# Performance work log

Measured on AMD Instinct MI355X. Metric: run time of the kernel, lower is better.

## Reference

```python
import jax, jax.numpy as jnp
import numpy as np

B, S, D, H, V, DFF = 8, 1024, 768, 12, 50257, 3072


def setup_inputs() -> dict:
    key = jax.random.key(0)
    ks = jax.random.split(key, 10)
    return {
        "idx": jax.random.randint(ks[0], (B, S), 0, V),
        "wte": jax.random.normal(ks[1], (V, D), jnp.float32) * 0.2,
        "wpe": jax.random.normal(ks[2], (S + 1, D), jnp.float32) * 0.2,
        "wq_diag": jax.random.normal(ks[3], (H, D), jnp.float32) * 0.2,
        "wk_diag": jax.random.normal(ks[4], (H, D), jnp.float32) * 0.2,
        "wv_diag": jax.random.normal(ks[5], (H, D), jnp.float32) * 0.2,
        "w_lr": jax.random.normal(ks[6], (1, H, 1, 1), jnp.float32) * 0.01,
        "w_o": jax.random.normal(ks[7], (D, H * D), jnp.float32) * 0.02,
        "mlp_w1": jax.random.normal(ks[8], (DFF, D), jnp.float32) * 0.02,
        "mlp_w2": jax.random.normal(ks[9], (D, DFF), jnp.float32) * 0.02,
    }


def _forward(idx, wte, wpe, wq_diag, wk_diag, wv_diag, w_lr, w_o, mlp_w1, mlp_w2):
    b_sz, s = idx.shape
    e = wte[idx]                               # (B,S,D) token embeddings
    p = wpe[: s + 1]                           # (S+1,D) positions 0..S
    e_mean = jnp.mean(wte, axis=0)             # E_wte: mean embedding (D,)
    invn = 1.0 / (jnp.arange(s, dtype=e.dtype) + 1.0)  # diag of W_N

    # diag-mode projections: (x @ diag(w)) == x * w  (per head)
    q = p[1:][None] * wq_diag[:, None, :]      # (H,S,D) -- batch-independent
    k = p[:-1][None] * wk_diag[:, None, :]     # (H,S,D)
    v = (e - e_mean)[:, None] * wv_diag[None, :, None, :]  # (B,H,S,D)

    scores = jnp.einsum("hsd,htd->hst", q, k)  # (H,S,S), identical per batch
    mask = jnp.tril(jnp.ones((s, s), bool))
    scores = jnp.where(mask, scores, -jnp.inf)
    attn = jax.nn.softmax(scores, axis=-1)
    y = jnp.einsum("hst,bhtd->bhsd", attn, v)  # (B,H,S,D)

    y = y * invn[:, None]                      # W_N @ y (diagonal -> row scale)
    y = y * w_lr                               # per-head W_LR scale
    # torch does y.view(B, S, H*D) on a (B,H,S,D) tensor: raw memory reinterpret
    y = y.reshape(b_sz, s, H * D)
    y = y @ w_o.T                              # W_o proj -> (B,S,D)

    # b = W_N @ (e - E_wte); torch broadcast-matmul then sum over dim=1 == batch
    b_term = (e - e_mean) * invn[None, :, None]        # (B,S,D)
    y = y + jnp.sum(b_term, axis=0)[None]              # (1,S,D) broadcast add

    # FFN block: x = x + mlp(x), GELU exact, no bias, dropout=0
    x = y + jax.nn.gelu(y @ mlp_w1.T, approximate=False) @ mlp_w2.T

    # targets=None path: logits only for last position, tied lm_head = wte
    logits = x[:, -1:, :] @ wte.T              # (B,1,V)
    return logits


def reference(idx, wte, wpe, wq_diag, wk_diag, wv_diag, w_lr, w_o, mlp_w1, mlp_w2):
    return _forward(idx, wte, wpe, wq_diag, wk_diag, wv_diag, w_lr, w_o, mlp_w1, mlp_w2)
```

## Files before the change

kernel.cpp:

```cpp
#include <hip/hip_runtime.h>
#include <math.h>

#define B 8
#define S 1024
#define D 768
#define H 12
#define V 50257
#define DFF 3072
#define HD (H*D)
#define SLO 1012
#define NS 12

#define OFF_EMEAN 0
#define OFF_A     768
#define OFF_GQ    (OFF_A + B*NS*D)
#define OFF_SC    (OFF_GQ + NS*D)
#define OFF_YV    (OFF_SC + NS*S)
#define OFF_YO    (OFF_YV + B*HD)
#define OFF_G     (OFF_YO + B*D)
#define OFF_X     (OFF_G + B*DFF)

typedef float f4 __attribute__((ext_vector_type(4)));

__device__ __forceinline__ float wsum(float v) {
    v += __shfl_xor(v, 1, 64);
    v += __shfl_xor(v, 2, 64);
    v += __shfl_xor(v, 4, 64);
    v += __shfl_xor(v, 8, 64);
    v += __shfl_xor(v, 16, 64);
    v += __shfl_xor(v, 32, 64);
    return v;
}

#define K14_K4_BLOCKS 256
#define K14_K1_BLOCKS 512
#define K1_ROWS 99
__global__ __launch_bounds__(768) void k14_emean_accA(const int* __restrict__ idx,
                                                      const float* __restrict__ wte,
                                                      float* __restrict__ ws) {
    __shared__ float wl[32 * 12];
    const int bid = blockIdx.x;
    const int tid = threadIdx.x;
    if (bid >= K14_K4_BLOCKS) {
        const int kb = bid - K14_K4_BLOCKS;
        int r0 = kb * K1_ROWS;
        if (r0 >= V) return;
        int r1 = r0 + K1_ROWS; if (r1 > V) r1 = V;
        const float* __restrict__ p = wte + (size_t)r0 * D + tid;
        float a0 = 0.f, a1 = 0.f, a2 = 0.f, a3 = 0.f;
        int r = r0;
        for (; r + 8 <= r1; r += 8) {
            const float* q0 = p;
            const float* q1 = p + 1 * D;
            const float* q2 = p + 2 * D;
            const float* q3 = p + 3 * D;
            const float* q4 = p + 4 * D;
            const float* q5 = p + 5 * D;
            const float* q6 = p + 6 * D;
            const float* q7 = p + 7 * D;
            float t0, t1, t2, t3, t4, t5, t6, t7;
            asm volatile("global_load_dword %0, %1, off" : "=v"(t0) : "v"(q0));
            asm volatile("global_load_dword %0, %1, off" : "=v"(t1) : "v"(q1));
            asm volatile("global_load_dword %0, %1, off" : "=v"(t2) : "v"(q2));
            asm volatile("global_load_dword %0, %1, off" : "=v"(t3) : "v"(q3));
            asm volatile("global_load_dword %0, %1, off" : "=v"(t4) : "v"(q4));
            asm volatile("global_load_dword %0, %1, off" : "=v"(t5) : "v"(q5));
            asm volatile("global_load_dword %0, %1, off" : "=v"(t6) : "v"(q6));
            asm volatile("global_load_dword %0, %1, off" : "=v"(t7) : "v"(q7));
            asm volatile("s_waitcnt vmcnt(0)"
                         : "+v"(t0), "+v"(t1), "+v"(t2), "+v"(t3),
                           "+v"(t4), "+v"(t5), "+v"(t6), "+v"(t7)
                         :
                         : "memory");
            __builtin_amdgcn_sched_barrier(0);
            a0 += t0 + t4; a1 += t1 + t5; a2 += t2 + t6; a3 += t3 + t7;
            p += 8 * D;
        }
        for (; r < r1; ++r) { a0 += *p; p += D; }
        atomicAdd(&ws[OFF_EMEAN + tid], a0 + a1 + a2 + a3);
    } else {
        const int tc = bid & 31, b = bid >> 5;
        if (tid < 384) {
            int tl = tid / 12, s12 = tid % 12;
            wl[tid] = ws[OFF_SC + s12 * S + tc * 32 + tl];
        }
        __syncthreads();
        float acc[12] = {0,0,0,0,0,0,0,0,0,0,0,0};
        const int* __restrict__ ib = idx + b * S + tc * 32;
#pragma unroll 4
        for (int tl = 0; tl < 32; ++tl) {
            int row = ib[tl];
            float val = wte[(size_t)row * D + tid];
            const float* w = &wl[tl * 12];
#pragma unroll
            for (int s12 = 0; s12 < 12; ++s12) acc[s12] += w[s12] * val;
        }
#pragma unroll
        for (int s12 = 0; s12 < 12; ++s12)
            atomicAdd(&ws[OFF_A + (b * NS + s12) * D + tid], acc[s12]);
    }
}

__global__ __launch_bounds__(256) void k2b_scores(const float* __restrict__ wpe,
                                                  const float* __restrict__ wq,
                                                  const float* __restrict__ wk,
                                                  float* __restrict__ ws) {
    const int lane = threadIdx.x & 63;
    const int t = (blockIdx.x * 256 + threadIdx.x) >> 6;
    float4 pw[3];
#pragma unroll
    for (int i = 0; i < 3; ++i) {
        int col = 4 * lane + 256 * i;
        float4 p = *reinterpret_cast<const float4*>(wpe + t * D + col);
        float4 q = *reinterpret_cast<const float4*>(wq + 11 * D + col);
        float4 k = *reinterpret_cast<const float4*>(wk + 11 * D + col);
        pw[i].x = p.x * q.x * k.x;
        pw[i].y = p.y * q.y * k.y;
        pw[i].z = p.z * q.z * k.z;
        pw[i].w = p.w * q.w * k.w;
    }
    float acc[12];
#pragma unroll
    for (int s12 = 0; s12 < 12; ++s12) {
        float a = 0.f;
#pragma unroll
        for (int i = 0; i < 3; ++i) {
            float4 g = *reinterpret_cast<const float4*>(wpe + (SLO + s12 + 1) * D + 4 * lane + 256 * i);
            a += pw[i].x * g.x + pw[i].y * g.y + pw[i].z * g.z + pw[i].w * g.w;
        }
        acc[s12] = a;
    }
#pragma unroll
    for (int s12 = 0; s12 < 12; ++s12) acc[s12] = wsum(acc[s12]);
    float v = acc[0];
#pragma unroll
    for (int j = 1; j < 12; ++j) if (lane == j) v = acc[j];
    if (lane < 12) ws[OFF_SC + lane * S + t] = v;
}

__global__ __launch_bounds__(256) void k3_softmax(float* __restrict__ ws) {
    __shared__ float red[256];
    const int s12 = blockIdx.x, tid = threadIdx.x;
    const int n = SLO + s12 + 1;
    float* sc = ws + OFF_SC + s12 * S;
    float m = -1e30f;
#pragma unroll
    for (int k = 0; k < 4; ++k) { int t = tid + 256 * k; if (t < n) m = fmaxf(m, sc[t]); }
    red[tid] = m; __syncthreads();
    for (int off = 128; off; off >>= 1) { if (tid < off) red[tid] = fmaxf(red[tid], red[tid + off]); __syncthreads(); }
    float mx = red[0]; __syncthreads();
    float sum = 0.f;
#pragma unroll
    for (int k = 0; k < 4; ++k) { int t = tid + 256 * k; if (t < n) sum += expf(sc[t] - mx); }
    red[tid] = sum; __syncthreads();
    for (int off = 128; off; off >>= 1) { if (tid < off) red[tid] += red[tid + off]; __syncthreads(); }
    float inv = 1.0f / red[0];
#pragma unroll
    for (int k = 0; k < 4; ++k) {
        int t = tid + 256 * k;
        sc[t] = (t < n) ? expf(sc[t] - mx) * inv : 0.0f;
    }
}

__global__ __launch_bounds__(256) void k5_yv(const int* __restrict__ idx,
                                             const float* __restrict__ wte,
                                             const float* __restrict__ wv,
                                             const float* __restrict__ wlr,
                                             float* __restrict__ ws) {
    if (blockIdx.x < 288) {
        int i = blockIdx.x * 256 + threadIdx.x;
        int b = i / HD, f = i % HD, s12 = f / D, d = f % D;
        float em = ws[OFF_EMEAN + d] * (1.0f / V);
        float A  = ws[OFF_A + (b * NS + s12) * D + d];
        float invn = 1.0f / (float)(SLO + s12 + 1);
        ws[OFF_YV + i] = (A - em) * wv[11 * D + d] * invn * wlr[11];
    } else {
        int d = (blockIdx.x - 288) * 256 + threadIdx.x;
        float em = ws[OFF_EMEAN + d] * (1.0f / V);
        float s = 0.f;
#pragma unroll
        for (int b = 0; b < 8; ++b) {
            int row = idx[b * S + (S - 1)];
            s += wte[(size_t)row * D + d];
        }
        float sb = (s - 8.0f * em) * (1.0f / (float)S);
#pragma unroll
        for (int b = 0; b < 8; ++b) ws[OFF_YO + b * D + d] = sb;
    }
}

__global__ __launch_bounds__(256) void k6_wo(const float* __restrict__ w_o,
                                             float* __restrict__ ws) {
    const int lane = threadIdx.x & 63;
    const int wid = (blockIdx.x * 256 + threadIdx.x) >> 6;
    const int kc = wid & 3;
    const int r0 = (wid >> 2) * 2;
    const int kbase = kc * 2304;
    float acc[2][8] = {{0}};
#pragma unroll
    for (int i = 0; i < 9; ++i) {
        int k = kbase + 4 * lane + 256 * i;
        float4 a0 = *reinterpret_cast<const float4*>(w_o + (size_t)r0 * HD + k);
        float4 a1 = *reinterpret_cast<const float4*>(w_o + (size_t)(r0 + 1) * HD + k);
#pragma unroll
        for (int b = 0; b < 8; ++b) {
            float4 y = *reinterpret_cast<const float4*>(ws + OFF_YV + b * HD + k);
            acc[0][b] += a0.x * y.x + a0.y * y.y + a0.z * y.z + a0.w * y.w;
            acc[1][b] += a1.x * y.x + a1.y * y.y + a1.z * y.z + a1.w * y.w;
        }
    }
#pragma unroll
    for (int r = 0; r < 2; ++r)
#pragma unroll
        for (int b = 0; b < 8; ++b) acc[r][b] = wsum(acc[r][b]);
    float v = acc[0][0];
#pragma unroll
    for (int l = 1; l < 16; ++l) if (lane == l) v = acc[l >> 3][l & 7];
    if (lane < 16) atomicAdd(&ws[OFF_YO + (lane & 7) * D + r0 + (lane >> 3)], v);
}

__global__ __launch_bounds__(256) void k7_mlp1(const float* __restrict__ w1,
                                               float* __restrict__ ws) {
    const int lane = threadIdx.x & 63;
    const int f = (blockIdx.x * 256 + threadIdx.x) >> 6;
    float acc[8] = {0};
#pragma unroll
    for (int i = 0; i < 3; ++i) {
        int dcol = 4 * lane + 256 * i;
        float4 w = *reinterpret_cast<const float4*>(w1 + (size_t)f * D + dcol);
#pragma unroll
        for (int b = 0; b < 8; ++b) {
            float4 y = *reinterpret_cast<const float4*>(ws + OFF_YO + b * D + dcol);
            acc[b] += w.x * y.x + w.y * y.y + w.z * y.z + w.w * y.w;
        }
    }
#pragma unroll
    for (int b = 0; b < 8; ++b) acc[b] = wsum(acc[b]);
    float v = acc[0];
#pragma unroll
    for (int j = 1; j < 8; ++j) if (lane == j) v = acc[j];
    if (lane < 8) {
        float g = 0.5f * v * (1.0f + erff(v * 0.70710678118654752f));
        ws[OFF_G + lane * DFF + f] = g;
    }
}

__global__ __launch_bounds__(256) void k8_mlp2(const float* __restrict__ w2,
                                               float* __restrict__ ws) {
    const int lane = threadIdx.x & 63;
    const int dd = (blockIdx.x * 256 + threadIdx.x) >> 6;
    float acc[8] = {0};
#pragma unroll
    for (int i = 0; i < 12; ++i) {
        int fcol = 4 * lane + 256 * i;
        float4 w = *reinterpret_cast<const float4*>(w2 + (size_t)dd * DFF + fcol);
#pragma unroll
        for (int b = 0; b < 8; ++b) {
            float4 g = *reinterpret_cast<const float4*>(ws + OFF_G + b * DFF + fcol);
            acc[b] += w.x * g.x + w.y * g.y + w.z * g.z + w.w * g.w;
        }
    }
#pragma unroll
    for (int b = 0; b < 8; ++b) acc[b] = wsum(acc[b]);
    float v = acc[0];
#pragma unroll
    for (int j = 1; j < 8; ++j) if (lane == j) v = acc[j];
    if (lane < 8) ws[OFF_X + lane * D + dd] = ws[OFF_YO + lane * D + dd] + v;
}

__global__ __launch_bounds__(256) void k9_logits(const float* __restrict__ wte,
                                                 const float* __restrict__ ws,
                                                 float* __restrict__ out) {
    const int lane = threadIdx.x & 63;
    const int wid = (blockIdx.x * 256 + threadIdx.x) >> 6;
    const int NW = gridDim.x * 4;
    float4 xr[8][3];
#pragma unroll
    for (int b = 0; b < 8; ++b)
#pragma unroll
        for (int i = 0; i < 3; ++i)
            xr[b][i] = *reinterpret_cast<const float4*>(ws + OFF_X + b * D + 4 * lane + 256 * i);
    int j = wid;
    float4 w[3];
    if (j < V) {
#pragma unroll
        for (int i = 0; i < 3; ++i)
            w[i] = *reinterpret_cast<const float4*>(wte + (size_t)j * D + 4 * lane + 256 * i);
    }
    while (j < V) {
        int jn = j + NW;
        float4 wn[3];
        if (jn < V) {
#pragma unroll
            for (int i = 0; i < 3; ++i)
                wn[i] = *reinterpret_cast<const float4*>(wte + (size_t)jn * D + 4 * lane + 256 * i);
        }
        float acc[8] = {0};
#pragma unroll
        for (int b = 0; b < 8; ++b) {
#pragma unroll
            for (int i = 0; i < 3; ++i)
                acc[b] += w[i].x * xr[b][i].x + w[i].y * xr[b][i].y +
                          w[i].z * xr[b][i].z + w[i].w * xr[b][i].w;
        }
#pragma unroll
        for (int b = 0; b < 8; ++b) acc[b] = wsum(acc[b]);
        float v = acc[0];
#pragma unroll
        for (int bb = 1; bb < 8; ++bb) if (lane == bb) v = acc[bb];
        if (lane < 8) out[(size_t)lane * V + j] = v;
#pragma unroll
        for (int i = 0; i < 3; ++i) w[i] = wn[i];
        j = jn;
    }
}

extern "C" void kernel_launch(void* const* d_in, const int* in_sizes, int n_in,
                              void* d_out, int out_size, void* d_ws, size_t ws_size,
                              hipStream_t stream) {
    const int*   idx = (const int*)  d_in[0];
    const float* wte = (const float*)d_in[1];
    const float* wpe = (const float*)d_in[2];
    const float* wq  = (const float*)d_in[3];
    const float* wk  = (const float*)d_in[4];
    const float* wv  = (const float*)d_in[5];
    const float* wlr = (const float*)d_in[6];
    const float* w_o = (const float*)d_in[7];
    const float* w1  = (const float*)d_in[8];
    const float* w2  = (const float*)d_in[9];
    float* out = (float*)d_out;
    float* ws  = (float*)d_ws;

    hipMemsetAsync(ws, 0, (size_t)(768 + B * NS * D) * sizeof(float), stream);

    k2b_scores<<<256, 256, 0, stream>>>(wpe, wq, wk, ws);
    k3_softmax<<<12,  256, 0, stream>>>(ws);
    k14_emean_accA<<<K14_K4_BLOCKS + K14_K1_BLOCKS, 768, 0, stream>>>(idx, wte, ws);
    k5_yv     <<<291, 256, 0, stream>>>(idx, wte, wv, wlr, ws);
    k6_wo     <<<384, 256, 0, stream>>>(w_o, ws);
    k7_mlp1   <<<768, 256, 0, stream>>>(w1, ws);
    k8_mlp2   <<<192, 256, 0, stream>>>(w2, ws);
    k9_logits <<<768, 256, 0, stream>>>(wte, ws, out);
}
```

Before: 352.6 us.

## Fold memset into score kernel, split-K w_o and mlp2, deepen logits prefetch

Drops the separate hipMemsetAsync and zeroes the emean/A region with extra blocks in the scores launch. The w_o and mlp2 GEMVs are split more finely along K (12-way and 4-way), which raises the block counts and merges partial sums with atomics. The residual copy into X moves into extra mlp1 blocks so that mlp2 can atomically add onto it. The logits loop prefetches two rows ahead instead of one. More atomics add contention and make summation order nondeterministic, and the extra register buffer in the logits kernel may lower occupancy.

```diff
diff --git a/kernel.cpp b/kernel.cpp
--- a/kernel.cpp
+++ b/kernel.cpp
@@ -101,10 +101,16 @@
     }
 }
 
+#define K2B_ZBLOCKS 291
 __global__ __launch_bounds__(256) void k2b_scores(const float* __restrict__ wpe,
                                                   const float* __restrict__ wq,
                                                   const float* __restrict__ wk,
                                                   float* __restrict__ ws) {
+    if (blockIdx.x >= 256) {
+        int i = (blockIdx.x - 256) * 256 + threadIdx.x;
+        ws[OFF_EMEAN + i] = 0.0f;
+        return;
+    }
     const int lane = threadIdx.x & 63;
     const int t = (blockIdx.x * 256 + threadIdx.x) >> 6;
     float4 pw[3];
@@ -193,12 +199,12 @@
                                              float* __restrict__ ws) {
     const int lane = threadIdx.x & 63;
     const int wid = (blockIdx.x * 256 + threadIdx.x) >> 6;
-    const int kc = wid & 3;
-    const int r0 = (wid >> 2) * 2;
-    const int kbase = kc * 2304;
+    const int kc = wid % 12;
+    const int r0 = (wid / 12) * 2;
+    const int kbase = kc * 768;
     float acc[2][8] = {{0}};
 #pragma unroll
-    for (int i = 0; i < 9; ++i) {
+    for (int i = 0; i < 3; ++i) {
         int k = kbase + 4 * lane + 256 * i;
         float4 a0 = *reinterpret_cast<const float4*>(w_o + (size_t)r0 * HD + k);
         float4 a1 = *reinterpret_cast<const float4*>(w_o + (size_t)(r0 + 1) * HD + k);
@@ -221,6 +227,11 @@
 
 __global__ __launch_bounds__(256) void k7_mlp1(const float* __restrict__ w1,
                                                float* __restrict__ ws) {
+    if (blockIdx.x >= 768) {
+        int i = (blockIdx.x - 768) * 256 + threadIdx.x;
+        ws[OFF_X + i] = ws[OFF_YO + i];
+        return;
+    }
     const int lane = threadIdx.x & 63;
     const int f = (blockIdx.x * 256 + threadIdx.x) >> 6;
     float acc[8] = {0};
@@ -248,11 +259,14 @@
 __global__ __launch_bounds__(256) void k8_mlp2(const float* __restrict__ w2,
                                                float* __restrict__ ws) {
     const int lane = threadIdx.x & 63;
-    const int dd = (blockIdx.x * 256 + threadIdx.x) >> 6;
+    const int wid = (blockIdx.x * 256 + threadIdx.x) >> 6;
+    const int fc = wid & 3;
+    const int dd = wid >> 2;
+    const int fbase = fc * 768;
     float acc[8] = {0};
 #pragma unroll
-    for (int i = 0; i < 12; ++i) {
-        int fcol = 4 * lane + 256 * i;
+    for (int i = 0; i < 3; ++i) {
+        int fcol = fbase + 4 * lane + 256 * i;
         float4 w = *reinterpret_cast<const float4*>(w2 + (size_t)dd * DFF + fcol);
 #pragma unroll
         for (int b = 0; b < 8; ++b) {
@@ -265,7 +279,7 @@
     float v = acc[0];
 #pragma unroll
     for (int j = 1; j < 8; ++j) if (lane == j) v = acc[j];
-    if (lane < 8) ws[OFF_X + lane * D + dd] = ws[OFF_YO + lane * D + dd] + v;
+    if (lane < 8) atomicAdd(&ws[OFF_X + lane * D + dd], v);
 }
 
 __global__ __launch_bounds__(256) void k9_logits(const float* __restrict__ wte,
@@ -280,28 +294,32 @@
 #pragma unroll
         for (int i = 0; i < 3; ++i)
             xr[b][i] = *reinterpret_cast<const float4*>(ws + OFF_X + b * D + 4 * lane + 256 * i);
-    int j = wid;
-    float4 w[3];
-    if (j < V) {
+    float4 w0[3], w1[3];
+    if (wid < V) {
 #pragma unroll
         for (int i = 0; i < 3; ++i)
-            w[i] = *reinterpret_cast<const float4*>(wte + (size_t)j * D + 4 * lane + 256 * i);
-    }
-    while (j < V) {
-        int jn = j + NW;
+            w0[i] = *reinterpret_cast<const float4*>(wte + (size_t)wid * D + 4 * lane + 256 * i);
+    }
+    if (wid + NW < V) {
+#pragma unroll
+        for (int i = 0; i < 3; ++i)
+            w1[i] = *reinterpret_cast<const float4*>(wte + (size_t)(wid + NW) * D + 4 * lane + 256 * i);
+    }
+    for (int j = wid; j < V; j += NW) {
+        int jn2 = j + 2 * NW;
         float4 wn[3];
-        if (jn < V) {
+        if (jn2 < V) {
 #pragma unroll
             for (int i = 0; i < 3; ++i)
-                wn[i] = *reinterpret_cast<const float4*>(wte + (size_t)jn * D + 4 * lane + 256 * i);
+                wn[i] = *reinterpret_cast<const float4*>(wte + (size_t)jn2 * D + 4 * lane + 256 * i);
         }
         float acc[8] = {0};
 #pragma unroll
         for (int b = 0; b < 8; ++b) {
 #pragma unroll
             for (int i = 0; i < 3; ++i)
-                acc[b] += w[i].x * xr[b][i].x + w[i].y * xr[b][i].y +
-                          w[i].z * xr[b][i].z + w[i].w * xr[b][i].w;
+                acc[b] += w0[i].x * xr[b][i].x + w0[i].y * xr[b][i].y +
+                          w0[i].z * xr[b][i].z + w0[i].w * xr[b][i].w;
         }
 #pragma unroll
         for (int b = 0; b < 8; ++b) acc[b] = wsum(acc[b]);
@@ -310,8 +328,7 @@
         for (int bb = 1; bb < 8; ++bb) if (lane == bb) v = acc[bb];
         if (lane < 8) out[(size_t)lane * V + j] = v;
 #pragma unroll
-        for (int i = 0; i < 3; ++i) w[i] = wn[i];
-        j = jn;
+        for (int i = 0; i < 3; ++i) { w0[i] = w1[i]; w1[i] = wn[i]; }
     }
 }
 
@@ -331,14 +348,12 @@
     float* out = (float*)d_out;
     float* ws  = (float*)d_ws;
 
-    hipMemsetAsync(ws, 0, (size_t)(768 + B * NS * D) * sizeof(float), stream);
-
-    k2b_scores<<<256, 256, 0, stream>>>(wpe, wq, wk, ws);
-    k3_softmax<<<12,  256, 0, stream>>>(ws);
+    k2b_scores<<<256 + K2B_ZBLOCKS, 256, 0, stream>>>(wpe, wq, wk, ws);
+    k3_softmax<<<12,   256, 0, stream>>>(ws);
     k14_emean_accA<<<K14_K4_BLOCKS + K14_K1_BLOCKS, 768, 0, stream>>>(idx, wte, ws);
-    k5_yv     <<<291, 256, 0, stream>>>(idx, wte, wv, wlr, ws);
-    k6_wo     <<<384, 256, 0, stream>>>(w_o, ws);
-    k7_mlp1   <<<768, 256, 0, stream>>>(w1, ws);
-    k8_mlp2   <<<192, 256, 0, stream>>>(w2, ws);
-    k9_logits <<<768, 256, 0, stream>>>(wte, ws, out);
-}
+    k5_yv     <<<291,  256, 0, stream>>>(idx, wte, wv, wlr, ws);
+    k6_wo     <<<1152, 256, 0, stream>>>(w_o, ws);
+    k7_mlp1   <<<792,  256, 0, stream>>>(w1, ws);
+    k8_mlp2   <<<768,  256, 0, stream>>>(w2, ws);
+    k9_logits <<<768,  256, 0, stream>>>(wte, ws, out);
+}
```

After: 337.0 us. 4.4% less time.
